# Performance work log

Measured on AMD Instinct MI355X. Metric: run time of the kernel, lower is better.

## Reference

```python
import jax, jax.numpy as jnp
import numpy as np

B, NELEC, D, NION = 2048, 32, 512, 8
NSPIN = 2
N = NELEC // NSPIN  # electrons per spin = orbital-matrix size = 16


def setup_inputs() -> dict:
    key = jax.random.key(0)
    ks = jax.random.split(key, 6)
    eq_inputs = jax.random.normal(ks[0], (B, NELEC, D), jnp.float32)
    r_ei = jax.random.normal(ks[1], (B, NELEC, NION, 3), jnp.float32)
    # learned params (stacked over the 2 spins; equal split so shapes match)
    W_lin = jax.random.normal(ks[2], (NSPIN, 2 * D, N), jnp.float32) * (0.5 / np.sqrt(D))
    b_lin = jax.random.normal(ks[3], (NSPIN, N), jnp.float32) * 0.1
    A_env = jax.random.normal(ks[4], (NSPIN, 3, 3, NION, N), jnp.float32) * 0.3
    w_ion = jax.random.normal(ks[5], (NSPIN, NION, N), jnp.float32)
    return dict(eq_inputs=eq_inputs, r_ei=r_ei, W_lin=W_lin, b_lin=b_lin,
                A_env=A_env, w_ion=w_ion)


def reference(eq_inputs, r_ei, W_lin, b_lin, A_env, w_ion):
    """Per-particle determinant antiequivariance layer.

    For each spin s and particle p, a doubly-equivariant orbital matrix
    M_p[j, k] = (y_p . W1[:,k] + y_j . W2[:,k] + b[k]) * env[j, k]
    is built (pair-concat dense split into two einsums to avoid the (B,n,n,2d)
    intermediate), with anisotropic exponential envelopes
    env[j, k] = sum_I w_ion[I,k] * exp(-||A[:,:,I,k] @ r_ei[j,I,:]||).
    Output per spin: y_p * det(M_p), stacked over spins -> (B, 2, n, d).
    """
    b, nelec, d = eq_inputs.shape
    n = nelec // NSPIN
    x = eq_inputs.reshape(b, NSPIN, n, d)            # spin_split=2 equal split
    r = r_ei.reshape(b, NSPIN, n, r_ei.shape[-2], 3)
    W1, W2 = W_lin[:, :d], W_lin[:, d:]
    # linear (doubly equivariant) part: (B, S, n_p, n_j, n_k)
    lin_p = jnp.einsum('bspf,sfk->bspk', x, W1)
    lin_j = jnp.einsum('bsjf,sfk->bsjk', x, W2) + b_lin[None, :, None, :]
    lin = lin_p[:, :, :, None, :] + lin_j[:, :, None, :, :]
    # anisotropic exponential envelopes: exp(-||A (r - R)||), combined over ions
    ar = jnp.einsum('bsjip,spqik->bsjiqk', r, A_env)        # (B,S,n,I,3,k)
    env = jnp.exp(-jnp.sqrt(jnp.sum(ar * ar, axis=-2)))     # (B,S,n,I,k)
    env = jnp.einsum('bsjik,sik->bsjk', env, w_ion)         # (B,S,n_j,n_k)
    M = lin * env[:, :, None, :, :]                         # (B,S,n_p,n_j,n_k)
    dets = jnp.linalg.det(M)                                # (B,S,n_p)
    # y_p * det(M_p), per spin (stacked over the spin axis)
    return x * dets[..., None]                              # (B,S,n,d)
```

## Files before the change

### kernel.cpp

```cpp
#include <hip/hip_runtime.h>
#include <cstdint>
#include <cstddef>

#define NSPIN 2
#define NPART 16
#define DDIM  512
#define NION  8

#define WB_FLOATS 8192
#define RS_OFF    8192
#define LINP_OFF  (RS_OFF + 1536)
#define LINJ_OFF  (LINP_OFF + 1024)
#define ENV_OFF   (LINJ_OFF + 1280)
#define DETS_OFF  (ENV_OFF + 1280)
#define LDS_FLOATS (DETS_OFF + 64)
#define LDS_BYTES  (LDS_FLOATS * 4)

typedef short bf16x8 __attribute__((ext_vector_type(8)));
typedef float f32x4  __attribute__((ext_vector_type(4)));

__device__ __forceinline__ short bfc(float x) {
    unsigned u = __float_as_uint(x);
    u += 0x7FFFu + ((u >> 16) & 1u);
    return (short)(u >> 16);
}

#define DPPMAXU(k, ctrl) { unsigned o_ = (unsigned)__builtin_amdgcn_update_dpp(0, (int)(k), (ctrl), 0xF, 0xF, true); (k) = (k) > o_ ? (k) : o_; }
#define DPPADDF(v, ctrl) { float o_ = __int_as_float(__builtin_amdgcn_update_dpp(0, __float_as_int(v), (ctrl), 0xF, 0xF, true)); (v) += o_; }

__global__ void __launch_bounds__(256, 3)
ppdet_kernel(const float* __restrict__ EQ, const float* __restrict__ RE,
             const float* __restrict__ WL, const float* __restrict__ BL,
             const float* __restrict__ AE, const float* __restrict__ WI,
             float* __restrict__ OUT)
{
    extern __shared__ float ls[];
    const int t  = threadIdx.x;
    const int s  = blockIdx.x >> 9;
    const int b0 = (blockIdx.x & 511) * 4;

    const int l  = t & 63;
    const int w  = t >> 6;
    const int c  = l & 15;
    const int h4 = l >> 4;
    const int jr = t & 15;
    const int ke = t >> 4;

    {
        const float* Wg = WL + (size_t)s * (2 * DDIM * NPART);
        ushort* wb = (ushort*)ls;
        #pragma unroll
        for (int it = 0; it < 8; ++it) {
            int slot = it * 256 + t;
            int half = slot >> 10;
            int ks   = (slot >> 6) & 15;
            int lane = slot & 63;
            int cc2  = lane & 15, hh = lane >> 4;
            const float* src = Wg + ((size_t)(half * 512 + ks * 32 + hh * 8)) * NPART + cc2;
            ushort u[8];
            #pragma unroll
            for (int e = 0; e < 8; ++e) u[e] = (ushort)bfc(src[e * NPART]);
            uint4 pk;
            pk.x = (unsigned)u[0] | ((unsigned)u[1] << 16);
            pk.y = (unsigned)u[2] | ((unsigned)u[3] << 16);
            pk.z = (unsigned)u[4] | ((unsigned)u[5] << 16);
            pk.w = (unsigned)u[6] | ((unsigned)u[7] << 16);
            *(uint4*)&wb[slot * 8] = pk;
        }
    }
    #pragma unroll
    for (int it = 0; it < 2; ++it) {
        int idx = it * 256 + t;
        if (idx < 384) {
            int bi = idx / 96, rem = idx % 96;
            ((float4*)(ls + RS_OFF))[idx] =
                ((const float4*)RE)[((size_t)(b0 + bi) * 32 + s * 16) * 6 + rem];
        }
    }
    __syncthreads();

    {
        const float* xg = EQ + ((size_t)(b0 + w) * 32 + s * 16 + c) * DDIM + h4 * 8;
        const ushort* wb = (const ushort*)ls;
        f32x4 accp = {0.f, 0.f, 0.f, 0.f}, accj = {0.f, 0.f, 0.f, 0.f};
        #pragma unroll
        for (int ks = 0; ks < 16; ++ks) {
            float4 a0 = *(const float4*)(xg + ks * 32);
            float4 a1 = *(const float4*)(xg + ks * 32 + 4);
            bf16x8 af;
            af[0] = bfc(a0.x); af[1] = bfc(a0.y); af[2] = bfc(a0.z); af[3] = bfc(a0.w);
            af[4] = bfc(a1.x); af[5] = bfc(a1.y); af[6] = bfc(a1.z); af[7] = bfc(a1.w);
            bf16x8 bf1 = *(const bf16x8*)(wb + (size_t)(ks * 64 + l) * 8);
            bf16x8 bf2 = *(const bf16x8*)(wb + (size_t)((16 + ks) * 64 + l) * 8);
            accp = __builtin_amdgcn_mfma_f32_16x16x32_bf16(af, bf1, accp, 0, 0, 0);
            accj = __builtin_amdgcn_mfma_f32_16x16x32_bf16(af, bf2, accj, 0, 0, 0);
        }
        const float blv = BL[s * NPART + c];
        #pragma unroll
        for (int q = 0; q < 4; ++q) {
            ls[LINP_OFF + (w * 16 + h4 * 4 + q) * 16 + c] = accp[q];
            ls[LINJ_OFF + (w * 16 + h4 * 4 + q) * 20 + c] = accj[q] + blv;
        }
    }

    {
        float G0[8], G1[8], G2[8], G3[8], G4[8], G5[8], wir[8];
        const float* Ag = AE + (size_t)s * (9 * NION * NPART);
        #pragma unroll
        for (int i = 0; i < 8; ++i) {
            float a00 = Ag[((0 * 3 + 0) * NION + i) * NPART + ke];
            float a01 = Ag[((0 * 3 + 1) * NION + i) * NPART + ke];
            float a02 = Ag[((0 * 3 + 2) * NION + i) * NPART + ke];
            float a10 = Ag[((1 * 3 + 0) * NION + i) * NPART + ke];
            float a11 = Ag[((1 * 3 + 1) * NION + i) * NPART + ke];
            float a12 = Ag[((1 * 3 + 2) * NION + i) * NPART + ke];
            float a20 = Ag[((2 * 3 + 0) * NION + i) * NPART + ke];
            float a21 = Ag[((2 * 3 + 1) * NION + i) * NPART + ke];
            float a22 = Ag[((2 * 3 + 2) * NION + i) * NPART + ke];
            G0[i] = a00 * a00 + a01 * a01 + a02 * a02;
            G1[i] = a10 * a10 + a11 * a11 + a12 * a12;
            G2[i] = a20 * a20 + a21 * a21 + a22 * a22;
            G3[i] = a00 * a10 + a01 * a11 + a02 * a12;
            G4[i] = a00 * a20 + a01 * a21 + a02 * a22;
            G5[i] = a10 * a20 + a11 * a21 + a12 * a22;
            wir[i] = WI[(size_t)s * (NION * NPART) + i * NPART + ke];
        }
        #pragma unroll
        for (int ib = 0; ib < 4; ++ib) {
            const float* rs = ls + RS_OFF + (ib * 16 + jr) * 24;
            float ev = 0.f;
            #pragma unroll
            for (int i = 0; i < 8; ++i) {
                float r0 = rs[i * 3], r1 = rs[i * 3 + 1], r2 = rs[i * 3 + 2];
                float ss = r0 * r0 * G0[i];
                ss = fmaf(r1 * r1, G1[i], ss);
                ss = fmaf(r2 * r2, G2[i], ss);
                float tcr = r0 * r1 * G3[i];
                tcr = fmaf(r0 * r2, G4[i], tcr);
                tcr = fmaf(r1 * r2, G5[i], tcr);
                ss = fmaf(2.f, tcr, ss);
                ss = fmaxf(ss, 0.f);
                ev = fmaf(wir[i], __expf(-__builtin_amdgcn_sqrtf(ss)), ev);
            }
            ls[ENV_OFF + (ib * 16 + jr) * 20 + ke] = ev;
        }
    }
    __syncthreads();

    for (int ib = 0; ib < 4; ++ib) {
        float Mr[16];
        const float* lp = ls + LINP_OFF + (ib * 16 + ke) * 16;
        const float* lj = ls + LINJ_OFF + (ib * 16 + jr) * 20;
        const float* ev = ls + ENV_OFF  + (ib * 16 + jr) * 20;
        #pragma unroll
        for (int cq = 0; cq < 4; ++cq) {
            float4 a = *(const float4*)(lp + cq * 4);
            float4 bb = *(const float4*)(lj + cq * 4);
            float4 e = *(const float4*)(ev + cq * 4);
            Mr[cq * 4 + 0] = (a.x + bb.x) * e.x;
            Mr[cq * 4 + 1] = (a.y + bb.y) * e.y;
            Mr[cq * 4 + 2] = (a.z + bb.z) * e.z;
            Mr[cq * 4 + 3] = (a.w + bb.w) * e.w;
        }
        float detv = 1.f;
        unsigned sel = 0u;
        int inv = 0;
        bool msel = false;
        #pragma unroll
        for (int cc = 0; cc < 16; ++cc) {
            unsigned key = msel ? 0u
                : ((__float_as_uint(fabsf(Mr[cc])) & 0xFFFFFFF0u) | (unsigned)jr);
            DPPMAXU(key, 0x121); DPPMAXU(key, 0x122); DPPMAXU(key, 0x124); DPPMAXU(key, 0x128);
            const int idx = (int)(key & 15u);
            const bool ispiv = (jr == idx);
            float Pr[16];
            #pragma unroll
            for (int k2 = cc; k2 < 16; ++k2) {
                float tt = ispiv ? Mr[k2] : 0.f;
                DPPADDF(tt, 0x121); DPPADDF(tt, 0x122); DPPADDF(tt, 0x124); DPPADDF(tt, 0x128);
                Pr[k2] = tt;
            }
            const float pv = Pr[cc];
            const float f = (msel || ispiv || pv == 0.f) ? 0.f
                          : Mr[cc] * __builtin_amdgcn_rcpf(pv);
            inv += __popc(sel >> (idx + 1));
            sel |= (1u << idx);
            msel = msel || ispiv;
            detv *= pv;
            #pragma unroll
            for (int k2 = cc + 1; k2 < 16; ++k2)
                Mr[k2] = fmaf(-f, Pr[k2], Mr[k2]);
        }
        if (inv & 1) detv = -detv;
        if (jr == 0) ls[DETS_OFF + ib * 16 + ke] = detv;
    }
    __syncthreads();

    #pragma unroll
    for (int ib = 0; ib < 4; ++ib) {
        const size_t base = ((size_t)(b0 + ib) * 32 + s * 16) * DDIM;
        #pragma unroll
        for (int i2 = 0; i2 < 8; ++i2) {
            int f4i = i2 * 256 + t;
            float dt = ls[DETS_OFF + ib * 16 + (f4i >> 7)];
            float4 xv = ((const float4*)(EQ + base))[f4i];
            float4 o = make_float4(xv.x * dt, xv.y * dt, xv.z * dt, xv.w * dt);
            ((float4*)(OUT + base))[f4i] = o;
        }
    }
}

extern "C" void kernel_launch(void* const* d_in, const int* in_sizes, int n_in,
                              void* d_out, int out_size, void* d_ws, size_t ws_size,
                              hipStream_t stream) {
    const float* EQ = (const float*)d_in[0];
    const float* RE = (const float*)d_in[1];
    const float* WL = (const float*)d_in[2];
    const float* BL = (const float*)d_in[3];
    const float* AE = (const float*)d_in[4];
    const float* WI = (const float*)d_in[5];
    float* OUT = (float*)d_out;
    (void)in_sizes; (void)n_in; (void)out_size; (void)d_ws; (void)ws_size;

    hipFuncSetAttribute((const void*)ppdet_kernel,
                        hipFuncAttributeMaxDynamicSharedMemorySize, LDS_BYTES);
    ppdet_kernel<<<dim3(1024), dim3(256), LDS_BYTES, stream>>>(EQ, RE, WL, BL, AE, WI, OUT);
}
```

Baseline: 87.60 us.

## Interleave four batch determinants and broadcast pivot rows via ds_bpermute

The pivot-row broadcast in the Gaussian elimination now uses one ds_bpermute per element from the pivot lane, replacing a masked four-step DPP add-reduction. The four batch items' eliminations are interleaved inside a single fully unrolled loop so their independent DPP and bpermute chains can overlap. The r_ei staging is also transposed in LDS to a component-major layout, making envelope reads conflict-free, at the cost of scalar rather than float4 global loads. Keeping a 4x16 matrix block live per thread raises register pressure, which may reduce occupancy or cause spills under the 3-block launch bound.

Measured after the change: 337.9 us. +285.8%, slower.

```diff
diff --git a/kernel.cpp b/kernel.cpp
--- a/kernel.cpp
+++ b/kernel.cpp
@@ -7,7 +7,6 @@
 #define DDIM  512
 #define NION  8
 
-#define WB_FLOATS 8192
 #define RS_OFF    8192
 #define LINP_OFF  (RS_OFF + 1536)
 #define LINJ_OFF  (LINP_OFF + 1024)
@@ -26,7 +25,6 @@
 }
 
 #define DPPMAXU(k, ctrl) { unsigned o_ = (unsigned)__builtin_amdgcn_update_dpp(0, (int)(k), (ctrl), 0xF, 0xF, true); (k) = (k) > o_ ? (k) : o_; }
-#define DPPADDF(v, ctrl) { float o_ = __int_as_float(__builtin_amdgcn_update_dpp(0, __float_as_int(v), (ctrl), 0xF, 0xF, true)); (v) += o_; }
 
 __global__ void __launch_bounds__(256, 3)
 ppdet_kernel(const float* __restrict__ EQ, const float* __restrict__ RE,
@@ -69,13 +67,11 @@
         }
     }
     #pragma unroll
-    for (int it = 0; it < 2; ++it) {
+    for (int it = 0; it < 6; ++it) {
         int idx = it * 256 + t;
-        if (idx < 384) {
-            int bi = idx / 96, rem = idx % 96;
-            ((float4*)(ls + RS_OFF))[idx] =
-                ((const float4*)RE)[((size_t)(b0 + bi) * 32 + s * 16) * 6 + rem];
-        }
+        int bi = idx / 384, rem = idx % 384;
+        int e = rem >> 4, j = rem & 15;
+        ls[RS_OFF + idx] = RE[((size_t)(b0 + bi) * 32 + s * 16 + j) * 24 + e];
     }
     __syncthreads();
 
@@ -127,11 +123,13 @@
         }
         #pragma unroll
         for (int ib = 0; ib < 4; ++ib) {
-            const float* rs = ls + RS_OFF + (ib * 16 + jr) * 24;
+            const float* rs = ls + RS_OFF + ib * 384;
             float ev = 0.f;
             #pragma unroll
             for (int i = 0; i < 8; ++i) {
-                float r0 = rs[i * 3], r1 = rs[i * 3 + 1], r2 = rs[i * 3 + 2];
+                float r0 = rs[(i * 3 + 0) * 16 + jr];
+                float r1 = rs[(i * 3 + 1) * 16 + jr];
+                float r2 = rs[(i * 3 + 2) * 16 + jr];
                 float ss = r0 * r0 * G0[i];
                 ss = fmaf(r1 * r1, G1[i], ss);
                 ss = fmaf(r2 * r2, G2[i], ss);
@@ -147,52 +145,71 @@
     }
     __syncthreads();
 
+    float Mr[4][16];
+    #pragma unroll
     for (int ib = 0; ib < 4; ++ib) {
-        float Mr[16];
         const float* lp = ls + LINP_OFF + (ib * 16 + ke) * 16;
         const float* lj = ls + LINJ_OFF + (ib * 16 + jr) * 20;
         const float* ev = ls + ENV_OFF  + (ib * 16 + jr) * 20;
         #pragma unroll
         for (int cq = 0; cq < 4; ++cq) {
-            float4 a = *(const float4*)(lp + cq * 4);
+            float4 a  = *(const float4*)(lp + cq * 4);
             float4 bb = *(const float4*)(lj + cq * 4);
-            float4 e = *(const float4*)(ev + cq * 4);
-            Mr[cq * 4 + 0] = (a.x + bb.x) * e.x;
-            Mr[cq * 4 + 1] = (a.y + bb.y) * e.y;
-            Mr[cq * 4 + 2] = (a.z + bb.z) * e.z;
-            Mr[cq * 4 + 3] = (a.w + bb.w) * e.w;
-        }
-        float detv = 1.f;
-        unsigned sel = 0u;
-        int inv = 0;
-        bool msel = false;
+            float4 e  = *(const float4*)(ev + cq * 4);
+            Mr[ib][cq * 4 + 0] = (a.x + bb.x) * e.x;
+            Mr[ib][cq * 4 + 1] = (a.y + bb.y) * e.y;
+            Mr[ib][cq * 4 + 2] = (a.z + bb.z) * e.z;
+            Mr[ib][cq * 4 + 3] = (a.w + bb.w) * e.w;
+        }
+    }
+    {
+        float detv[4] = {1.f, 1.f, 1.f, 1.f};
+        unsigned sel[4] = {0u, 0u, 0u, 0u};
+        int inv[4] = {0, 0, 0, 0};
+        bool msel[4] = {false, false, false, false};
+        const int lanebase4 = (t & 48) << 2;
         #pragma unroll
         for (int cc = 0; cc < 16; ++cc) {
-            unsigned key = msel ? 0u
-                : ((__float_as_uint(fabsf(Mr[cc])) & 0xFFFFFFF0u) | (unsigned)jr);
-            DPPMAXU(key, 0x121); DPPMAXU(key, 0x122); DPPMAXU(key, 0x124); DPPMAXU(key, 0x128);
-            const int idx = (int)(key & 15u);
-            const bool ispiv = (jr == idx);
-            float Pr[16];
-            #pragma unroll
-            for (int k2 = cc; k2 < 16; ++k2) {
-                float tt = ispiv ? Mr[k2] : 0.f;
-                DPPADDF(tt, 0x121); DPPADDF(tt, 0x122); DPPADDF(tt, 0x124); DPPADDF(tt, 0x128);
-                Pr[k2] = tt;
+            unsigned key[4];
+            #pragma unroll
+            for (int ib = 0; ib < 4; ++ib)
+                key[ib] = msel[ib] ? 0u
+                    : ((__float_as_uint(fabsf(Mr[ib][cc])) & 0xFFFFFFF0u) | (unsigned)jr);
+            #pragma unroll
+            for (int ib = 0; ib < 4; ++ib) { DPPMAXU(key[ib], 0x121); }
+            #pragma unroll
+            for (int ib = 0; ib < 4; ++ib) { DPPMAXU(key[ib], 0x122); }
+            #pragma unroll
+            for (int ib = 0; ib < 4; ++ib) { DPPMAXU(key[ib], 0x124); }
+            #pragma unroll
+            for (int ib = 0; ib < 4; ++ib) { DPPMAXU(key[ib], 0x128); }
+            #pragma unroll
+            for (int ib = 0; ib < 4; ++ib) {
+                const int idx = (int)(key[ib] & 15u);
+                const bool ispiv = (jr == idx) && !msel[ib];
+                const int srcaddr = lanebase4 | (idx << 2);
+                float Pr[16];
+                #pragma unroll
+                for (int k2 = cc; k2 < 16; ++k2)
+                    Pr[k2] = __int_as_float(__builtin_amdgcn_ds_bpermute(
+                                 srcaddr, __float_as_int(Mr[ib][k2])));
+                const float pv = Pr[cc];
+                const float f = (msel[ib] || ispiv || pv == 0.f) ? 0.f
+                              : Mr[ib][cc] * __builtin_amdgcn_rcpf(pv);
+                inv[ib] += __popc(sel[ib] >> (idx + 1));
+                sel[ib] |= (1u << idx);
+                msel[ib] = msel[ib] || ispiv;
+                detv[ib] *= pv;
+                #pragma unroll
+                for (int k2 = cc + 1; k2 < 16; ++k2)
+                    Mr[ib][k2] = fmaf(-f, Pr[k2], Mr[ib][k2]);
             }
-            const float pv = Pr[cc];
-            const float f = (msel || ispiv || pv == 0.f) ? 0.f
-                          : Mr[cc] * __builtin_amdgcn_rcpf(pv);
-            inv += __popc(sel >> (idx + 1));
-            sel |= (1u << idx);
-            msel = msel || ispiv;
-            detv *= pv;
-            #pragma unroll
-            for (int k2 = cc + 1; k2 < 16; ++k2)
-                Mr[k2] = fmaf(-f, Pr[k2], Mr[k2]);
-        }
-        if (inv & 1) detv = -detv;
-        if (jr == 0) ls[DETS_OFF + ib * 16 + ke] = detv;
+        }
+        #pragma unroll
+        for (int ib = 0; ib < 4; ++ib) {
+            if (inv[ib] & 1) detv[ib] = -detv[ib];
+            if (jr == 0) ls[DETS_OFF + ib * 16 + ke] = detv[ib];
+        }
     }
     __syncthreads();
 
```
